# Optimization experiments

Hardware: AMD Instinct MI355X
Metric: run time of the kernel (lower is better)

## Reference

```python
import jax, jax.numpy as jnp
import numpy as np
from jax import lax

DN = ('NCHW', 'OIHW', 'NCHW')

def conv(x, w, b, stride):
    y = lax.conv_general_dilated(x, w, window_strides=(stride, stride),
                                 padding='VALID', dimension_numbers=DN)
    return y + b[None, :, None, None]

def setup_inputs() -> dict:
    key = jax.random.key(0)
    ks = jax.random.split(key, 7)
    B = 4096
    def he(k, shape, fan_in):
        return jax.random.normal(k, shape, jnp.float32) * np.sqrt(2.0 / fan_in)
    return {
        'x':  jax.random.normal(ks[0], (B, 3, 48, 64), jnp.float32),
        'w1': he(ks[1], (32, 3, 8, 8), 3 * 8 * 8),
        'b1': jnp.zeros((32,), jnp.float32),
        'w2': he(ks[2], (64, 32, 3, 3), 32 * 3 * 3),
        'b2': jnp.zeros((64,), jnp.float32),
        'w3': he(ks[3], (64, 64, 3, 3), 64 * 3 * 3),
        'b3': jnp.zeros((64,), jnp.float32),
        'w4': he(ks[4], (512, 960), 960),
        'b4': jnp.zeros((512,), jnp.float32),
        'w5': he(ks[5], (2, 512), 512),
        'b5': jnp.zeros((2,), jnp.float32),
    }

def reference(x, w1, b1, w2, b2, w3, b3, w4, b4, w5, b5):
    # conv1 (k8 s4): [B,3,48,64] -> [B,32,11,15]
    x1 = conv(x, w1, b1, 4)
    # side reduction (torch code does this on CPU with python loops):
    # sum over batch and channel dims of pre-ReLU activation, divided by 32
    ave1 = jnp.sum(x1, axis=(0, 1)) / 32.0          # [11,15]
    x2 = jax.nn.relu(x1)
    # conv2 (k3 s2): -> [B,64,5,7]
    x3 = conv(x2, w2, b2, 2)
    ave2 = jnp.sum(x3, axis=(0, 1)) / 64.0          # [5,7]
    x4 = jax.nn.relu(x3)
    # conv3 (k3 s1): -> [B,64,3,5]
    x5 = conv(x4, w3, b3, 1)
    ave3 = jnp.sum(x5, axis=(0, 1)) / 64.0          # [3,5]
    x6 = jax.nn.relu(x5)
    # fc head: flatten (C,H,W order, matching torch) -> 960 -> 512 -> 2
    h = x6.reshape(x6.shape[0], -1)                 # [B,960]
    h = jax.nn.relu(h @ w4.T + b4)
    out = h @ w5.T + b5                             # [B,2]
    return out, ave1, ave2, ave3
```

## Files before the change

### kernel.cpp

```cpp
#include <hip/hip_runtime.h>
#include <hip/hip_bf16.h>

#define BATCH 4096

typedef __attribute__((ext_vector_type(8))) short short8;
typedef __attribute__((ext_vector_type(4))) float f32x4;

#define MFMA_BF16 __builtin_amdgcn_mfma_f32_16x16x32_bf16

__device__ __forceinline__ float frelu(float v) { return v > 0.f ? v : 0.f; }
__device__ __forceinline__ unsigned short f2bf(float f) {
    return __builtin_bit_cast(unsigned short, __float2bfloat16(f));
}
__device__ __forceinline__ short8 cvt8(const float* p) {
    float4 a = *(const float4*)p;
    float4 b = *(const float4*)(p + 4);
    short8 r;
    r[0] = (short)f2bf(a.x); r[1] = (short)f2bf(a.y); r[2] = (short)f2bf(a.z); r[3] = (short)f2bf(a.w);
    r[4] = (short)f2bf(b.x); r[5] = (short)f2bf(b.y); r[6] = (short)f2bf(b.z); r[7] = (short)f2bf(b.w);
    return r;
}

__global__ __launch_bounds__(256) void prep_kernel(const float* __restrict__ w2, const float* __restrict__ w3,
                                                   const float* __restrict__ w4, const float* __restrict__ b5,
                                                   unsigned short* __restrict__ w2p, unsigned short* __restrict__ w3p,
                                                   unsigned short* __restrict__ w4p, float* __restrict__ out) {
    int idx = blockIdx.x * 256 + threadIdx.x;
    if (idx < 18432) {
        int oc = idx / 288, k = idx % 288;
        int khw = k / 32, ic = k % 32;
        w2p[idx] = f2bf(w2[oc * 288 + ic * 9 + khw]);
    } else if (idx < 55296) {
        int j = idx - 18432;
        int oc = j / 576, k = j % 576;
        int khw = k / 64, ic = k % 64;
        w3p[j] = f2bf(w3[oc * 576 + ic * 9 + khw]);
    } else if (idx < 546816) {
        int j = idx - 55296;
        int n = j / 960, k = j % 960;
        int pos = k / 64, oc = k % 64;
        w4p[j] = f2bf(w4[n * 960 + oc * 15 + pos]);
    } else if (idx < 555008) {
        int j = idx - 546816;
        out[j] = b5[j & 1];
    } else if (idx < 555223) {
        out[8192 + (idx - 555008)] = 0.f;
    }
}

__global__ __launch_bounds__(256) void conv1_mfma(const float* __restrict__ x,
                                                  const float* __restrict__ w1, const float* __restrict__ b1,
                                                  unsigned short* __restrict__ x2, float* __restrict__ red1) {
    __shared__ float red[176];
    const int img = blockIdx.x;
    const int tid = threadIdx.x;
    const int wave = tid >> 6, lane = tid & 63;
    const int col = lane & 15, quad = lane >> 4;
    if (tid < 176) red[tid] = 0.f;

    short8 Bf[2][6];
    #pragma unroll
    for (int nt = 0; nt < 2; ++nt) {
        const int oc = nt * 16 + col;
        #pragma unroll
        for (int c = 0; c < 6; ++c)
            Bf[nt][c] = cvt8(w1 + oc * 192 + c * 32 + quad * 8);
    }
    const float bias0 = b1[col], bias1 = b1[col + 16];
    __syncthreads();

    const float* ximg = x + (size_t)img * 9216;
    #pragma unroll
    for (int ti = 0; ti < 3; ++ti) {
        const int t = wave + ti * 4;
        if (t >= 11) break;
        const int posA = t * 16 + col;
        const int pm = posA < 165 ? posA : 164;
        const int oh = pm / 15, ow = pm % 15;
        f32x4 acc0 = {0.f, 0.f, 0.f, 0.f}, acc1 = {0.f, 0.f, 0.f, 0.f};
        #pragma unroll
        for (int c = 0; c < 6; ++c) {
            const int ic = c >> 1;
            const int kh = (c & 1) * 4 + quad;
            const float* ap = ximg + (ic * 48 + oh * 4 + kh) * 64 + ow * 4;
            short8 af = cvt8(ap);
            acc0 = MFMA_BF16(af, Bf[0][c], acc0, 0, 0, 0);
            acc1 = MFMA_BF16(af, Bf[1][c], acc1, 0, 0, 0);
        }
        #pragma unroll
        for (int r = 0; r < 4; ++r) {
            const int pr = t * 16 + quad * 4 + r;
            float v0 = acc0[r] + bias0;
            float v1 = acc1[r] + bias1;
            float s = v0 + v1;
            s += __shfl_xor(s, 1); s += __shfl_xor(s, 2);
            s += __shfl_xor(s, 4); s += __shfl_xor(s, 8);
            if (pr < 165) {
                if (col == 0) atomicAdd(&red[pr], s);
                unsigned short* dst = x2 + ((size_t)img * 165 + pr) * 32;
                dst[col]      = f2bf(frelu(v0));
                dst[col + 16] = f2bf(frelu(v1));
            }
        }
    }
    __syncthreads();
    if (tid < 176) red1[(size_t)tid * 4096 + img] = red[tid];
}

__global__ __launch_bounds__(256) void reduce1_kernel(const float* __restrict__ red1, float* __restrict__ ave1) {
    const int pos = blockIdx.x;
    float s = 0.f;
    for (int i = threadIdx.x; i < 4096; i += 256) s += red1[(size_t)pos * 4096 + i];
    s += __shfl_down(s, 32); s += __shfl_down(s, 16); s += __shfl_down(s, 8);
    s += __shfl_down(s, 4);  s += __shfl_down(s, 2);  s += __shfl_down(s, 1);
    __shared__ float wsum[4];
    if ((threadIdx.x & 63) == 0) wsum[threadIdx.x >> 6] = s;
    __syncthreads();
    if (threadIdx.x == 0) ave1[pos] = (wsum[0] + wsum[1] + wsum[2] + wsum[3]) * 0.03125f;
}

__global__ __launch_bounds__(256) void conv2_mfma(const unsigned short* __restrict__ x2,
                                                  const unsigned short* __restrict__ w2p, const float* __restrict__ b2,
                                                  unsigned short* __restrict__ x4, float* __restrict__ ave2) {
    __shared__ unsigned short wl[64 * 296];
    __shared__ float red[35];
    const int tid = threadIdx.x;
    {
        const float4* src = (const float4*)w2p;
        for (int i = tid; i < 2304; i += 256) {
            int row = i / 36, off = i % 36;
            *(float4*)((char*)wl + row * 592 + off * 16) = src[i];
        }
    }
    if (tid < 35) red[tid] = 0.f;
    __syncthreads();

    const int wave = tid >> 6, lane = tid & 63;
    const int col = lane & 15, quad = lane >> 4;
    const int tile0 = blockIdx.x * 16 + wave * 4;

    const unsigned short* abase[4];
    #pragma unroll
    for (int mi = 0; mi < 4; ++mi) {
        const int m = (tile0 + mi) * 16 + col;
        const int b = m / 35, pos = m % 35;
        const int oh = pos / 7, ow = pos % 7;
        abase[mi] = x2 + ((size_t)b * 165 + oh * 30 + ow * 2) * 32 + quad * 8;
    }
    f32x4 acc[4][4] = {};
    #pragma unroll
    for (int c = 0; c < 9; ++c) {
        const int kh = c / 3, kw = c % 3;
        short8 Bf[4];
        #pragma unroll
        for (int nt = 0; nt < 4; ++nt)
            Bf[nt] = *(const short8*)((const char*)wl + ((nt * 16 + col) * 296 + c * 32 + quad * 8) * 2);
        #pragma unroll
        for (int mi = 0; mi < 4; ++mi) {
            short8 af = *(const short8*)(abase[mi] + (kh * 15 + kw) * 32);
            #pragma unroll
            for (int nt = 0; nt < 4; ++nt)
                acc[mi][nt] = MFMA_BF16(af, Bf[nt], acc[mi][nt], 0, 0, 0);
        }
    }
    float bv[4];
    #pragma unroll
    for (int nt = 0; nt < 4; ++nt) bv[nt] = b2[nt * 16 + col];
    #pragma unroll
    for (int mi = 0; mi < 4; ++mi) {
        const int mrow0 = (tile0 + mi) * 16;
        #pragma unroll
        for (int r = 0; r < 4; ++r) {
            const int m = mrow0 + quad * 4 + r;
            const int b = m / 35, pos = m % 35;
            unsigned short* dst = x4 + ((size_t)b * 35 + pos) * 64;
            float s = 0.f;
            #pragma unroll
            for (int nt = 0; nt < 4; ++nt) {
                float v = acc[mi][nt][r] + bv[nt];
                s += v;
                dst[nt * 16 + col] = f2bf(frelu(v));
            }
            s += __shfl_xor(s, 1); s += __shfl_xor(s, 2); s += __shfl_xor(s, 4); s += __shfl_xor(s, 8);
            if (col == 0) atomicAdd(&red[pos], s);
        }
    }
    __syncthreads();
    if (tid < 35) atomicAdd(&ave2[tid], red[tid] * 0.015625f);
}

__global__ __launch_bounds__(256) void conv3_mfma(const unsigned short* __restrict__ x4,
                                                  const unsigned short* __restrict__ w3p, const float* __restrict__ b3,
                                                  unsigned short* __restrict__ x6, float* __restrict__ ave3) {
    __shared__ unsigned short wl[32 * 584];
    __shared__ float red[15];
    const int tid = threadIdx.x;
    const int oc0 = blockIdx.y * 32;
    {
        const float4* src = (const float4*)(w3p + (size_t)oc0 * 576);
        for (int i = tid; i < 2304; i += 256) {
            int row = i / 72, off = i % 72;
            *(float4*)((char*)wl + row * 1168 + off * 16) = src[i];
        }
    }
    if (tid < 15) red[tid] = 0.f;
    __syncthreads();

    const int wave = tid >> 6, lane = tid & 63;
    const int col = lane & 15, quad = lane >> 4;
    const int tile0 = blockIdx.x * 16 + wave * 4;

    const unsigned short* abase[4];
    #pragma unroll
    for (int mi = 0; mi < 4; ++mi) {
        const int m = (tile0 + mi) * 16 + col;
        const int b = m / 15, pos = m % 15;
        const int oh = pos / 5, ow = pos % 5;
        abase[mi] = x4 + ((size_t)b * 35 + oh * 7 + ow) * 64 + quad * 8;
    }
    f32x4 acc[4][2] = {};
    #pragma unroll
    for (int c = 0; c < 18; ++c) {
        const int khw = c >> 1, kh = khw / 3, kw = khw % 3;
        const int icoff = (c & 1) * 32;
        short8 Bf[2];
        #pragma unroll
        for (int nt = 0; nt < 2; ++nt)
            Bf[nt] = *(const short8*)((const char*)wl + ((nt * 16 + col) * 584 + c * 32 + quad * 8) * 2);
        #pragma unroll
        for (int mi = 0; mi < 4; ++mi) {
            short8 af = *(const short8*)(abase[mi] + (kh * 7 + kw) * 64 + icoff);
            #pragma unroll
            for (int nt = 0; nt < 2; ++nt)
                acc[mi][nt] = MFMA_BF16(af, Bf[nt], acc[mi][nt], 0, 0, 0);
        }
    }
    float bv[2];
    #pragma unroll
    for (int nt = 0; nt < 2; ++nt) bv[nt] = b3[oc0 + nt * 16 + col];
    #pragma unroll
    for (int mi = 0; mi < 4; ++mi) {
        const int mrow0 = (tile0 + mi) * 16;
        #pragma unroll
        for (int r = 0; r < 4; ++r) {
            const int m = mrow0 + quad * 4 + r;
            const int b = m / 15, pos = m % 15;
            unsigned short* dst = x6 + (size_t)b * 960 + pos * 64 + oc0;
            float s = 0.f;
            #pragma unroll
            for (int nt = 0; nt < 2; ++nt) {
                float v = acc[mi][nt][r] + bv[nt];
                s += v;
                dst[nt * 16 + col] = f2bf(frelu(v));
            }
            s += __shfl_xor(s, 1); s += __shfl_xor(s, 2); s += __shfl_xor(s, 4); s += __shfl_xor(s, 8);
            if (col == 0) atomicAdd(&red[pos], s);
        }
    }
    __syncthreads();
    if (tid < 15) atomicAdd(&ave3[tid], red[tid] * 0.015625f);
}

__global__ __launch_bounds__(256) void fc4_mfma(const unsigned short* __restrict__ x6,
                                                const unsigned short* __restrict__ w4p, const float* __restrict__ b4,
                                                const float* __restrict__ w5, float* __restrict__ out) {
    const int tid = threadIdx.x;
    const int wave = tid >> 6, lane = tid & 63;
    const int col = lane & 15, quad = lane >> 4;
    const int m0 = blockIdx.x * 128 + wave * 32;
    const int n0 = blockIdx.y * 64;

    const unsigned short* arow0 = x6 + (size_t)(m0 + col) * 960 + quad * 8;
    const unsigned short* arow1 = arow0 + 16 * 960;
    f32x4 acc[2][4] = {};
    for (int c = 0; c < 30; ++c) {
        short8 Bf[4];
        #pragma unroll
        for (int nt = 0; nt < 4; ++nt)
            Bf[nt] = *(const short8*)(w4p + (size_t)(n0 + nt * 16 + col) * 960 + c * 32 + quad * 8);
        short8 a0 = *(const short8*)(arow0 + c * 32);
        short8 a1 = *(const short8*)(arow1 + c * 32);
        #pragma unroll
        for (int nt = 0; nt < 4; ++nt) {
            acc[0][nt] = MFMA_BF16(a0, Bf[nt], acc[0][nt], 0, 0, 0);
            acc[1][nt] = MFMA_BF16(a1, Bf[nt], acc[1][nt], 0, 0, 0);
        }
    }
    float bv[4], w50[4], w51[4];
    #pragma unroll
    for (int nt = 0; nt < 4; ++nt) {
        const int oc = n0 + nt * 16 + col;
        bv[nt] = b4[oc]; w50[nt] = w5[oc]; w51[nt] = w5[512 + oc];
    }
    #pragma unroll
    for (int mi = 0; mi < 2; ++mi) {
        #pragma unroll
        for (int r = 0; r < 4; ++r) {
            float l0 = 0.f, l1 = 0.f;
            #pragma unroll
            for (int nt = 0; nt < 4; ++nt) {
                float hh = frelu(acc[mi][nt][r] + bv[nt]);
                l0 += hh * w50[nt];
                l1 += hh * w51[nt];
            }
            l0 += __shfl_xor(l0, 1); l0 += __shfl_xor(l0, 2); l0 += __shfl_xor(l0, 4); l0 += __shfl_xor(l0, 8);
            l1 += __shfl_xor(l1, 1); l1 += __shfl_xor(l1, 2); l1 += __shfl_xor(l1, 4); l1 += __shfl_xor(l1, 8);
            if (col == 0) {
                const int gm = m0 + mi * 16 + quad * 4 + r;
                atomicAdd(&out[gm * 2 + 0], l0);
                atomicAdd(&out[gm * 2 + 1], l1);
            }
        }
    }
}

extern "C" void kernel_launch(void* const* d_in, const int* in_sizes, int n_in,
                              void* d_out, int out_size, void* d_ws, size_t ws_size,
                              hipStream_t stream) {
    const float* x  = (const float*)d_in[0];
    const float* w1 = (const float*)d_in[1];
    const float* b1 = (const float*)d_in[2];
    const float* w2 = (const float*)d_in[3];
    const float* b2 = (const float*)d_in[4];
    const float* w3 = (const float*)d_in[5];
    const float* b3 = (const float*)d_in[6];
    const float* w4 = (const float*)d_in[7];
    const float* b4 = (const float*)d_in[8];
    const float* w5 = (const float*)d_in[9];
    const float* b5 = (const float*)d_in[10];
    float* out = (float*)d_out;

    unsigned short* ws = (unsigned short*)d_ws;
    unsigned short* x2  = ws;
    unsigned short* x4  = ws + 21626880;
    unsigned short* x6  = ws + 30801920;
    unsigned short* w2p = ws + 34734080;
    unsigned short* w3p = ws + 34752512;
    unsigned short* w4p = ws + 34789376;
    float* red1 = (float*)((char*)d_ws + 70561792);

    float* ave1 = out + 8192;
    float* ave2 = out + 8192 + 165;
    float* ave3 = out + 8192 + 200;

    prep_kernel<<<2169, 256, 0, stream>>>(w2, w3, w4, b5, w2p, w3p, w4p, out);
    conv1_mfma<<<BATCH, 256, 0, stream>>>(x, w1, b1, x2, red1);
    reduce1_kernel<<<165, 256, 0, stream>>>(red1, ave1);
    conv2_mfma<<<560, 256, 0, stream>>>(x2, w2p, b2, x4, ave2);
    conv3_mfma<<<dim3(240, 2), 256, 0, stream>>>(x4, w3p, b3, x6, ave3);
    fc4_mfma<<<dim3(32, 8), 256, 0, stream>>>(x6, w4p, b4, w5, out);
}
```

Measured before the change: 364.5 us.

## Stage conv1 input and fc4 weights in LDS; halve conv2/conv3 tiles for more blocks

conv1 now copies each image into padded shared memory with coalesced float4 loads, so the strided im2col reads hit LDS instead of global memory. conv2 and conv3 process half as many M-tiles per wave and launch twice as many blocks, which gives more parallelism at the cost of reloading weights into LDS more often. fc4 stages a 32-column slice of w4 into LDS and doubles the grid along N, which reduces B-fragment global loads but reads the x6 activations twice as many times.

```diff
diff --git a/kernel.cpp b/kernel.cpp
--- a/kernel.cpp
+++ b/kernel.cpp
@@ -51,11 +51,18 @@
 __global__ __launch_bounds__(256) void conv1_mfma(const float* __restrict__ x,
                                                   const float* __restrict__ w1, const float* __restrict__ b1,
                                                   unsigned short* __restrict__ x2, float* __restrict__ red1) {
+    __shared__ float xs[3 * 48 * 68];
     __shared__ float red[176];
     const int img = blockIdx.x;
     const int tid = threadIdx.x;
     const int wave = tid >> 6, lane = tid & 63;
     const int col = lane & 15, quad = lane >> 4;
+
+    const float4* xg = (const float4*)(x + (size_t)img * 9216);
+    for (int i = tid; i < 2304; i += 256) {
+        int row = i >> 4, seg = i & 15;
+        *(float4*)(xs + row * 68 + seg * 4) = xg[row * 16 + seg];
+    }
     if (tid < 176) red[tid] = 0.f;
 
     short8 Bf[2][6];
@@ -69,7 +76,6 @@
     const float bias0 = b1[col], bias1 = b1[col + 16];
     __syncthreads();
 
-    const float* ximg = x + (size_t)img * 9216;
     #pragma unroll
     for (int ti = 0; ti < 3; ++ti) {
         const int t = wave + ti * 4;
@@ -82,7 +88,7 @@
         for (int c = 0; c < 6; ++c) {
             const int ic = c >> 1;
             const int kh = (c & 1) * 4 + quad;
-            const float* ap = ximg + (ic * 48 + oh * 4 + kh) * 64 + ow * 4;
+            const float* ap = xs + ic * 3264 + (oh * 4 + kh) * 68 + ow * 4;
             short8 af = cvt8(ap);
             acc0 = MFMA_BF16(af, Bf[0][c], acc0, 0, 0, 0);
             acc1 = MFMA_BF16(af, Bf[1][c], acc1, 0, 0, 0);
@@ -137,17 +143,17 @@
 
     const int wave = tid >> 6, lane = tid & 63;
     const int col = lane & 15, quad = lane >> 4;
-    const int tile0 = blockIdx.x * 16 + wave * 4;
-
-    const unsigned short* abase[4];
-    #pragma unroll
-    for (int mi = 0; mi < 4; ++mi) {
+    const int tile0 = blockIdx.x * 8 + wave * 2;
+
+    const unsigned short* abase[2];
+    #pragma unroll
+    for (int mi = 0; mi < 2; ++mi) {
         const int m = (tile0 + mi) * 16 + col;
         const int b = m / 35, pos = m % 35;
         const int oh = pos / 7, ow = pos % 7;
         abase[mi] = x2 + ((size_t)b * 165 + oh * 30 + ow * 2) * 32 + quad * 8;
     }
-    f32x4 acc[4][4] = {};
+    f32x4 acc[2][4] = {};
     #pragma unroll
     for (int c = 0; c < 9; ++c) {
         const int kh = c / 3, kw = c % 3;
@@ -156,7 +162,7 @@
         for (int nt = 0; nt < 4; ++nt)
             Bf[nt] = *(const short8*)((const char*)wl + ((nt * 16 + col) * 296 + c * 32 + quad * 8) * 2);
         #pragma unroll
-        for (int mi = 0; mi < 4; ++mi) {
+        for (int mi = 0; mi < 2; ++mi) {
             short8 af = *(const short8*)(abase[mi] + (kh * 15 + kw) * 32);
             #pragma unroll
             for (int nt = 0; nt < 4; ++nt)
@@ -167,7 +173,7 @@
     #pragma unroll
     for (int nt = 0; nt < 4; ++nt) bv[nt] = b2[nt * 16 + col];
     #pragma unroll
-    for (int mi = 0; mi < 4; ++mi) {
+    for (int mi = 0; mi < 2; ++mi) {
         const int mrow0 = (tile0 + mi) * 16;
         #pragma unroll
         for (int r = 0; r < 4; ++r) {
@@ -208,17 +214,17 @@
 
     const int wave = tid >> 6, lane = tid & 63;
     const int col = lane & 15, quad = lane >> 4;
-    const int tile0 = blockIdx.x * 16 + wave * 4;
-
-    const unsigned short* abase[4];
-    #pragma unroll
-    for (int mi = 0; mi < 4; ++mi) {
+    const int tile0 = blockIdx.x * 8 + wave * 2;
+
+    const unsigned short* abase[2];
+    #pragma unroll
+    for (int mi = 0; mi < 2; ++mi) {
         const int m = (tile0 + mi) * 16 + col;
         const int b = m / 15, pos = m % 15;
         const int oh = pos / 5, ow = pos % 5;
         abase[mi] = x4 + ((size_t)b * 35 + oh * 7 + ow) * 64 + quad * 8;
     }
-    f32x4 acc[4][2] = {};
+    f32x4 acc[2][2] = {};
     #pragma unroll
     for (int c = 0; c < 18; ++c) {
         const int khw = c >> 1, kh = khw / 3, kw = khw % 3;
@@ -228,7 +234,7 @@
         for (int nt = 0; nt < 2; ++nt)
             Bf[nt] = *(const short8*)((const char*)wl + ((nt * 16 + col) * 584 + c * 32 + quad * 8) * 2);
         #pragma unroll
-        for (int mi = 0; mi < 4; ++mi) {
+        for (int mi = 0; mi < 2; ++mi) {
             short8 af = *(const short8*)(abase[mi] + (kh * 7 + kw) * 64 + icoff);
             #pragma unroll
             for (int nt = 0; nt < 2; ++nt)
@@ -239,7 +245,7 @@
     #pragma unroll
     for (int nt = 0; nt < 2; ++nt) bv[nt] = b3[oc0 + nt * 16 + col];
     #pragma unroll
-    for (int mi = 0; mi < 4; ++mi) {
+    for (int mi = 0; mi < 2; ++mi) {
         const int mrow0 = (tile0 + mi) * 16;
         #pragma unroll
         for (int r = 0; r < 4; ++r) {
@@ -264,32 +270,42 @@
 __global__ __launch_bounds__(256) void fc4_mfma(const unsigned short* __restrict__ x6,
                                                 const unsigned short* __restrict__ w4p, const float* __restrict__ b4,
                                                 const float* __restrict__ w5, float* __restrict__ out) {
+    __shared__ unsigned short wl[32 * 968];
     const int tid = threadIdx.x;
     const int wave = tid >> 6, lane = tid & 63;
     const int col = lane & 15, quad = lane >> 4;
-    const int m0 = blockIdx.x * 128 + wave * 32;
-    const int n0 = blockIdx.y * 64;
-
-    const unsigned short* arow0 = x6 + (size_t)(m0 + col) * 960 + quad * 8;
+    const int m0 = blockIdx.x * 128;
+    const int oc0 = blockIdx.y * 32;
+
+    {
+        const float4* src = (const float4*)(w4p + (size_t)oc0 * 960);
+        for (int i = tid; i < 3840; i += 256) {
+            int row = i / 120, seg = i % 120;
+            *(float4*)((char*)wl + row * 1936 + seg * 16) = src[i];
+        }
+    }
+    __syncthreads();
+
+    const unsigned short* arow0 = x6 + (size_t)(m0 + wave * 32 + col) * 960 + quad * 8;
     const unsigned short* arow1 = arow0 + 16 * 960;
-    f32x4 acc[2][4] = {};
+    f32x4 acc[2][2] = {};
     for (int c = 0; c < 30; ++c) {
-        short8 Bf[4];
-        #pragma unroll
-        for (int nt = 0; nt < 4; ++nt)
-            Bf[nt] = *(const short8*)(w4p + (size_t)(n0 + nt * 16 + col) * 960 + c * 32 + quad * 8);
+        short8 Bf[2];
+        #pragma unroll
+        for (int nt = 0; nt < 2; ++nt)
+            Bf[nt] = *(const short8*)((const char*)wl + ((nt * 16 + col) * 968 + c * 32 + quad * 8) * 2);
         short8 a0 = *(const short8*)(arow0 + c * 32);
         short8 a1 = *(const short8*)(arow1 + c * 32);
         #pragma unroll
-        for (int nt = 0; nt < 4; ++nt) {
+        for (int nt = 0; nt < 2; ++nt) {
             acc[0][nt] = MFMA_BF16(a0, Bf[nt], acc[0][nt], 0, 0, 0);
             acc[1][nt] = MFMA_BF16(a1, Bf[nt], acc[1][nt], 0, 0, 0);
         }
     }
-    float bv[4], w50[4], w51[4];
-    #pragma unroll
-    for (int nt = 0; nt < 4; ++nt) {
-        const int oc = n0 + nt * 16 + col;
+    float bv[2], w50[2], w51[2];
+    #pragma unroll
+    for (int nt = 0; nt < 2; ++nt) {
+        const int oc = oc0 + nt * 16 + col;
         bv[nt] = b4[oc]; w50[nt] = w5[oc]; w51[nt] = w5[512 + oc];
     }
     #pragma unroll
@@ -298,7 +314,7 @@
         for (int r = 0; r < 4; ++r) {
             float l0 = 0.f, l1 = 0.f;
             #pragma unroll
-            for (int nt = 0; nt < 4; ++nt) {
+            for (int nt = 0; nt < 2; ++nt) {
                 float hh = frelu(acc[mi][nt][r] + bv[nt]);
                 l0 += hh * w50[nt];
                 l1 += hh * w51[nt];
@@ -306,7 +322,7 @@
             l0 += __shfl_xor(l0, 1); l0 += __shfl_xor(l0, 2); l0 += __shfl_xor(l0, 4); l0 += __shfl_xor(l0, 8);
             l1 += __shfl_xor(l1, 1); l1 += __shfl_xor(l1, 2); l1 += __shfl_xor(l1, 4); l1 += __shfl_xor(l1, 8);
             if (col == 0) {
-                const int gm = m0 + mi * 16 + quad * 4 + r;
+                const int gm = m0 + wave * 32 + mi * 16 + quad * 4 + r;
                 atomicAdd(&out[gm * 2 + 0], l0);
                 atomicAdd(&out[gm * 2 + 1], l1);
             }
@@ -346,7 +362,7 @@
     prep_kernel<<<2169, 256, 0, stream>>>(w2, w3, w4, b5, w2p, w3p, w4p, out);
     conv1_mfma<<<BATCH, 256, 0, stream>>>(x, w1, b1, x2, red1);
     reduce1_kernel<<<165, 256, 0, stream>>>(red1, ave1);
-    conv2_mfma<<<560, 256, 0, stream>>>(x2, w2p, b2, x4, ave2);
-    conv3_mfma<<<dim3(240, 2), 256, 0, stream>>>(x4, w3p, b3, x6, ave3);
-    fc4_mfma<<<dim3(32, 8), 256, 0, stream>>>(x6, w4p, b4, w5, out);
-}
+    conv2_mfma<<<1120, 256, 0, stream>>>(x2, w2p, b2, x4, ave2);
+    conv3_mfma<<<dim3(480, 2), 256, 0, stream>>>(x4, w3p, b3, x6, ave3);
+    fc4_mfma<<<dim3(32, 16), 256, 0, stream>>>(x6, w4p, b4, w5, out);
+}
```

New measurement: 379.6 us. +4.1%, slower.
